# Kernel tuning notes

Measured on AMD Instinct MI355X. Metric: run time of the kernel, lower is better.

The kernel has to match this reference:

```python
import jax, jax.numpy as jnp
import numpy as np

NUM_TOKENS = 16384
HIDDEN = 2048
NUM_EXPERTS = 64
TOP_K = 2


def setup_inputs() -> dict:
    key = jax.random.key(0)
    kx, kw = jax.random.split(key)
    x = jax.random.normal(kx, (NUM_TOKENS, HIDDEN), dtype=jnp.float32)
    # nn.Linear weight is (num_experts, hidden); store transposed for x @ W
    W_gate = jax.random.normal(kw, (HIDDEN, NUM_EXPERTS), dtype=jnp.float32) * (1.0 / np.sqrt(HIDDEN))
    return {"x": x, "W_gate": W_gate}


def reference(x, W_gate):
    # gate matmul + softmax over experts
    logits = jnp.einsum("th,he->te", x, W_gate)          # (T, E)
    probs = jax.nn.softmax(logits, axis=-1)
    # top-k selection and renormalization
    top_k_weights, top_k_indices = jax.lax.top_k(probs, TOP_K)  # (T, k), (T, k)
    top_k_weights = top_k_weights / (jnp.sum(top_k_weights, axis=-1, keepdims=True) + 1e-9)
    # Switch-style load-balancing aux loss using top-1 assignments
    num_tokens = x.shape[0]
    top1 = top_k_indices[:, 0]
    tokens_per_expert = jnp.zeros((NUM_EXPERTS,), dtype=probs.dtype).at[top1].add(1.0)
    f = tokens_per_expert / num_tokens                    # fraction of tokens per expert
    P = jnp.mean(probs, axis=0)                           # mean router prob per expert
    aux_loss = NUM_EXPERTS * jnp.sum(f * P)
    return (top_k_weights, top_k_indices, aux_loss)
```

## Files before the change

### kernel.cpp

```cpp
#include <hip/hip_runtime.h>
#include <math.h>

#define NUM_TOKENS 16384
#define HIDDEN 2048
#define NUM_EXPERTS 64
#define TOPK 2

#define TM 64
#define KH 64
#define XS_STR 68

#define IDX_OFF 32768
#define AUX_OFF 65536

__global__ __launch_bounds__(256) void router_kernel(
    const float* __restrict__ x, const float* __restrict__ Wg,
    float* __restrict__ out, float* __restrict__ ws)
{
    __shared__ float sA[TM * XS_STR];
    __shared__ float sB[KH * NUM_EXPERTS];

    const int tid = threadIdx.x;
    const int bid = blockIdx.x;
    const int tx = tid & 15;
    const int ty = tid >> 4;
    const int tokBase = bid * TM;

    float C[4][4] = {{0.f,0.f,0.f,0.f},{0.f,0.f,0.f,0.f},{0.f,0.f,0.f,0.f},{0.f,0.f,0.f,0.f}};

    for (int hb = 0; hb < HIDDEN; hb += KH) {
        #pragma unroll
        for (int p = 0; p < 4; ++p) {
            int li = p * 256 + tid;
            int t  = li >> 4;
            int hq = li & 15;
            float4 v = *reinterpret_cast<const float4*>(
                &x[(size_t)(tokBase + t) * HIDDEN + hb + hq * 4]);
            *reinterpret_cast<float4*>(&sA[t * XS_STR + hq * 4]) = v;
        }
        #pragma unroll
        for (int p = 0; p < 4; ++p) {
            int li = p * 256 + tid;
            float4 v = *reinterpret_cast<const float4*>(
                &Wg[(size_t)hb * NUM_EXPERTS + li * 4]);
            *reinterpret_cast<float4*>(&sB[li * 4]) = v;
        }
        __syncthreads();

        #pragma unroll
        for (int k4 = 0; k4 < KH / 4; ++k4) {
            float xa[4][4];
            float wa[4][4];
            #pragma unroll
            for (int i = 0; i < 4; ++i) {
                float4 v = *reinterpret_cast<const float4*>(
                    &sA[(ty * 4 + i) * XS_STR + k4 * 4]);
                xa[i][0] = v.x; xa[i][1] = v.y; xa[i][2] = v.z; xa[i][3] = v.w;
            }
            #pragma unroll
            for (int kk = 0; kk < 4; ++kk) {
                float4 v = *reinterpret_cast<const float4*>(
                    &sB[(k4 * 4 + kk) * NUM_EXPERTS + tx * 4]);
                wa[kk][0] = v.x; wa[kk][1] = v.y; wa[kk][2] = v.z; wa[kk][3] = v.w;
            }
            #pragma unroll
            for (int i = 0; i < 4; ++i)
                #pragma unroll
                for (int kk = 0; kk < 4; ++kk)
                    #pragma unroll
                    for (int jj = 0; jj < 4; ++jj)
                        C[i][jj] = fmaf(xa[i][kk], wa[kk][jj], C[i][jj]);
        }
        __syncthreads();
    }

    #pragma unroll
    for (int i = 0; i < 4; ++i) {
        float4 v; v.x = C[i][0]; v.y = C[i][1]; v.z = C[i][2]; v.w = C[i][3];
        *reinterpret_cast<float4*>(&sA[(ty * 4 + i) * XS_STR + tx * 4]) = v;
    }
    __syncthreads();

    const int wave = tid >> 6;
    const int lane = tid & 63;
    float accP = 0.f;
    float accC = 0.f;

    for (int tt = 0; tt < TM / 4; ++tt) {
        int t = wave * (TM / 4) + tt;
        float l = sA[t * XS_STR + lane];

        float m = l;
        #pragma unroll
        for (int off = 32; off >= 1; off >>= 1) m = fmaxf(m, __shfl_xor(m, off));
        float p = expf(l - m);
        float Z = p;
        #pragma unroll
        for (int off = 32; off >= 1; off >>= 1) Z += __shfl_xor(Z, off);
        float prob = p / Z;

        float v1 = prob; int i1 = lane;
        #pragma unroll
        for (int off = 32; off >= 1; off >>= 1) {
            float ov = __shfl_xor(v1, off);
            int   oi = __shfl_xor(i1, off);
            if (ov > v1 || (ov == v1 && oi < i1)) { v1 = ov; i1 = oi; }
        }
        float v2 = (lane == i1) ? -1.f : prob; int i2 = lane;
        #pragma unroll
        for (int off = 32; off >= 1; off >>= 1) {
            float ov = __shfl_xor(v2, off);
            int   oi = __shfl_xor(i2, off);
            if (ov > v2 || (ov == v2 && oi < i2)) { v2 = ov; i2 = oi; }
        }

        accP += prob;
        if (lane == i1) accC += 1.f;

        if (lane == 0) {
            float s = v1 + v2 + 1e-9f;
            size_t o = (size_t)(tokBase + t) * 2;
            out[o]               = v1 / s;
            out[o + 1]           = v2 / s;
            out[IDX_OFF + o]     = (float)i1;
            out[IDX_OFF + o + 1] = (float)i2;
        }
    }

    sB[wave * 64 + lane]       = accP;
    sB[256 + wave * 64 + lane] = accC;
    __syncthreads();
    if (tid < 64) {
        float sp = sB[tid] + sB[64 + tid] + sB[128 + tid] + sB[192 + tid];
        float sc = sB[256 + tid] + sB[320 + tid] + sB[384 + tid] + sB[448 + tid];
        ws[(size_t)bid * 128 + tid]      = sp;
        ws[(size_t)bid * 128 + 64 + tid] = sc;
    }
}

__global__ __launch_bounds__(64) void finalize_kernel(
    const float* __restrict__ ws, float* __restrict__ out)
{
    int e = threadIdx.x;
    float sp = 0.f, sc = 0.f;
    for (int b = 0; b < NUM_TOKENS / TM; ++b) {
        sp += ws[(size_t)b * 128 + e];
        sc += ws[(size_t)b * 128 + 64 + e];
    }
    float val = (sc * (1.0f / NUM_TOKENS)) * (sp * (1.0f / NUM_TOKENS));
    #pragma unroll
    for (int off = 32; off >= 1; off >>= 1) val += __shfl_xor(val, off);
    if (e == 0) out[AUX_OFF] = (float)NUM_EXPERTS * val;
}

extern "C" void kernel_launch(void* const* d_in, const int* in_sizes, int n_in,
                              void* d_out, int out_size, void* d_ws, size_t ws_size,
                              hipStream_t stream) {
    const float* x  = (const float*)d_in[0];
    const float* Wg = (const float*)d_in[1];
    float* out = (float*)d_out;
    float* ws  = (float*)d_ws;

    router_kernel<<<NUM_TOKENS / TM, 256, 0, stream>>>(x, Wg, out, ws);
    finalize_kernel<<<1, 64, 0, stream>>>(ws, out);
}
```

Before: 116.6 us.

## Restructure router GEMM as per-token split-K with wave-uniform weight loads

Each thread now owns one token and accumulates all 64 expert logits in registers. Eight waves each take a 256-wide slice of the hidden dimension and read the gate weights with wave-uniform (scalar/broadcast) loads instead of staging them in shared memory. Partial sums are combined through a shared-memory tree reduction, and softmax/top-2 run per thread without cross-lane shuffles. The goal is to remove LDS staging and shuffle overhead. In exchange, x is read with strided per-thread rows (poor coalescing), register pressure rises (64 accumulators), and grid parallelism is limited to 256 blocks.

```diff
diff --git a/kernel.cpp b/kernel.cpp
--- a/kernel.cpp
+++ b/kernel.cpp
@@ -4,146 +4,132 @@
 #define NUM_TOKENS 16384
 #define HIDDEN 2048
 #define NUM_EXPERTS 64
-#define TOPK 2
-
-#define TM 64
-#define KH 64
-#define XS_STR 68
 
 #define IDX_OFF 32768
 #define AUX_OFF 65536
 
-__global__ __launch_bounds__(256) void router_kernel(
+#define KSLICE 256
+
+__global__ __launch_bounds__(512) void router_kernel(
     const float* __restrict__ x, const float* __restrict__ Wg,
     float* __restrict__ out, float* __restrict__ ws)
 {
-    __shared__ float sA[TM * XS_STR];
-    __shared__ float sB[KH * NUM_EXPERTS];
+    __shared__ float buf[4][64][68];
+    __shared__ int top1s[64];
 
-    const int tid = threadIdx.x;
-    const int bid = blockIdx.x;
-    const int tx = tid & 15;
-    const int ty = tid >> 4;
-    const int tokBase = bid * TM;
+    const int tid  = threadIdx.x;
+    const int w    = tid >> 6;
+    const int lane = tid & 63;
+    const int token = blockIdx.x * 64 + lane;
 
-    float C[4][4] = {{0.f,0.f,0.f,0.f},{0.f,0.f,0.f,0.f},{0.f,0.f,0.f,0.f},{0.f,0.f,0.f,0.f}};
+    const int k0 = __builtin_amdgcn_readfirstlane(w) * KSLICE;
 
-    for (int hb = 0; hb < HIDDEN; hb += KH) {
+    float C[64];
+    #pragma unroll
+    for (int e = 0; e < 64; ++e) C[e] = 0.f;
+
+    const float4* xr = reinterpret_cast<const float4*>(x + (size_t)token * HIDDEN + k0);
+
+    float4 xc[4], xn[4];
+    #pragma unroll
+    for (int j = 0; j < 4; ++j) xc[j] = xr[j];
+
+    for (int c = 0; c < 16; ++c) {
+        if (c < 15) {
+            #pragma unroll
+            for (int j = 0; j < 4; ++j) xn[j] = xr[(c + 1) * 4 + j];
+        }
+        const int kbase = k0 + c * 16;
         #pragma unroll
-        for (int p = 0; p < 4; ++p) {
-            int li = p * 256 + tid;
-            int t  = li >> 4;
-            int hq = li & 15;
-            float4 v = *reinterpret_cast<const float4*>(
-                &x[(size_t)(tokBase + t) * HIDDEN + hb + hq * 4]);
-            *reinterpret_cast<float4*>(&sA[t * XS_STR + hq * 4]) = v;
+        for (int j = 0; j < 4; ++j) {
+            const float xv[4] = {xc[j].x, xc[j].y, xc[j].z, xc[j].w};
+            #pragma unroll
+            for (int q = 0; q < 4; ++q) {
+                const int k = kbase + j * 4 + q;
+                const float4* wr = reinterpret_cast<const float4*>(Wg + (size_t)k * NUM_EXPERTS);
+                #pragma unroll
+                for (int e4 = 0; e4 < 16; ++e4) {
+                    const float4 wv = wr[e4];
+                    C[e4*4+0] = fmaf(xv[q], wv.x, C[e4*4+0]);
+                    C[e4*4+1] = fmaf(xv[q], wv.y, C[e4*4+1]);
+                    C[e4*4+2] = fmaf(xv[q], wv.z, C[e4*4+2]);
+                    C[e4*4+3] = fmaf(xv[q], wv.w, C[e4*4+3]);
+                }
+            }
         }
-        #pragma unroll
-        for (int p = 0; p < 4; ++p) {
-            int li = p * 256 + tid;
-            float4 v = *reinterpret_cast<const float4*>(
-                &Wg[(size_t)hb * NUM_EXPERTS + li * 4]);
-            *reinterpret_cast<float4*>(&sB[li * 4]) = v;
+        if (c < 15) {
+            #pragma unroll
+            for (int j = 0; j < 4; ++j) xc[j] = xn[j];
         }
-        __syncthreads();
-
-        #pragma unroll
-        for (int k4 = 0; k4 < KH / 4; ++k4) {
-            float xa[4][4];
-            float wa[4][4];
-            #pragma unroll
-            for (int i = 0; i < 4; ++i) {
-                float4 v = *reinterpret_cast<const float4*>(
-                    &sA[(ty * 4 + i) * XS_STR + k4 * 4]);
-                xa[i][0] = v.x; xa[i][1] = v.y; xa[i][2] = v.z; xa[i][3] = v.w;
-            }
-            #pragma unroll
-            for (int kk = 0; kk < 4; ++kk) {
-                float4 v = *reinterpret_cast<const float4*>(
-                    &sB[(k4 * 4 + kk) * NUM_EXPERTS + tx * 4]);
-                wa[kk][0] = v.x; wa[kk][1] = v.y; wa[kk][2] = v.z; wa[kk][3] = v.w;
-            }
-            #pragma unroll
-            for (int i = 0; i < 4; ++i)
-                #pragma unroll
-                for (int kk = 0; kk < 4; ++kk)
-                    #pragma unroll
-                    for (int jj = 0; jj < 4; ++jj)
-                        C[i][jj] = fmaf(xa[i][kk], wa[kk][jj], C[i][jj]);
-        }
-        __syncthreads();
     }
 
-    #pragma unroll
-    for (int i = 0; i < 4; ++i) {
-        float4 v; v.x = C[i][0]; v.y = C[i][1]; v.z = C[i][2]; v.w = C[i][3];
-        *reinterpret_cast<float4*>(&sA[(ty * 4 + i) * XS_STR + tx * 4]) = v;
+    #define WBUF(b) { _Pragma("unroll") for (int e4 = 0; e4 < 16; ++e4) { \
+        float4 v; v.x = C[e4*4+0]; v.y = C[e4*4+1]; v.z = C[e4*4+2]; v.w = C[e4*4+3]; \
+        *reinterpret_cast<float4*>(&buf[b][lane][e4*4]) = v; } }
+    #define ABUF(b) { _Pragma("unroll") for (int e4 = 0; e4 < 16; ++e4) { \
+        const float4 v = *reinterpret_cast<const float4*>(&buf[b][lane][e4*4]); \
+        C[e4*4+0] += v.x; C[e4*4+1] += v.y; C[e4*4+2] += v.z; C[e4*4+3] += v.w; } }
+
+    if (w >= 4) WBUF(w - 4);
+    __syncthreads();
+    if (w < 4) ABUF(w);
+    __syncthreads();
+    if (w == 2 || w == 3) WBUF(w - 2);
+    __syncthreads();
+    if (w < 2) ABUF(w);
+    __syncthreads();
+    if (w == 1) WBUF(0);
+    __syncthreads();
+
+    if (w == 0) {
+        ABUF(0);
+
+        float m = C[0];
+        #pragma unroll
+        for (int e = 1; e < 64; ++e) m = fmaxf(m, C[e]);
+        float Z = 0.f;
+        #pragma unroll
+        for (int e = 0; e < 64; ++e) { C[e] = expf(C[e] - m); Z += C[e]; }
+        const float rz = 1.f / Z;
+
+        float v1 = -1.f, v2 = -1.f; int i1 = 0, i2 = 0;
+        #pragma unroll
+        for (int e = 0; e < 64; ++e) {
+            const float p = C[e] * rz;
+            C[e] = p;
+            if (p > v1)      { v2 = v1; i2 = i1; v1 = p; i1 = e; }
+            else if (p > v2) { v2 = p;  i2 = e; }
+        }
+
+        const float s = v1 + v2 + 1e-9f;
+        float2 wo; wo.x = v1 / s; wo.y = v2 / s;
+        *reinterpret_cast<float2*>(&out[(size_t)token * 2]) = wo;
+        float2 io; io.x = (float)i1; io.y = (float)i2;
+        *reinterpret_cast<float2*>(&out[IDX_OFF + (size_t)token * 2]) = io;
+
+        WBUF(0);
+        top1s[lane] = i1;
     }
     __syncthreads();
 
-    const int wave = tid >> 6;
-    const int lane = tid & 63;
-    float accP = 0.f;
-    float accC = 0.f;
-
-    for (int tt = 0; tt < TM / 4; ++tt) {
-        int t = wave * (TM / 4) + tt;
-        float l = sA[t * XS_STR + lane];
-
-        float m = l;
-        #pragma unroll
-        for (int off = 32; off >= 1; off >>= 1) m = fmaxf(m, __shfl_xor(m, off));
-        float p = expf(l - m);
-        float Z = p;
-        #pragma unroll
-        for (int off = 32; off >= 1; off >>= 1) Z += __shfl_xor(Z, off);
-        float prob = p / Z;
-
-        float v1 = prob; int i1 = lane;
-        #pragma unroll
-        for (int off = 32; off >= 1; off >>= 1) {
-            float ov = __shfl_xor(v1, off);
-            int   oi = __shfl_xor(i1, off);
-            if (ov > v1 || (ov == v1 && oi < i1)) { v1 = ov; i1 = oi; }
-        }
-        float v2 = (lane == i1) ? -1.f : prob; int i2 = lane;
-        #pragma unroll
-        for (int off = 32; off >= 1; off >>= 1) {
-            float ov = __shfl_xor(v2, off);
-            int   oi = __shfl_xor(i2, off);
-            if (ov > v2 || (ov == v2 && oi < i2)) { v2 = ov; i2 = oi; }
-        }
-
-        accP += prob;
-        if (lane == i1) accC += 1.f;
-
-        if (lane == 0) {
-            float s = v1 + v2 + 1e-9f;
-            size_t o = (size_t)(tokBase + t) * 2;
-            out[o]               = v1 / s;
-            out[o + 1]           = v2 / s;
-            out[IDX_OFF + o]     = (float)i1;
-            out[IDX_OFF + o + 1] = (float)i2;
-        }
-    }
-
-    sB[wave * 64 + lane]       = accP;
-    sB[256 + wave * 64 + lane] = accC;
-    __syncthreads();
-    if (tid < 64) {
-        float sp = sB[tid] + sB[64 + tid] + sB[128 + tid] + sB[192 + tid];
-        float sc = sB[256 + tid] + sB[320 + tid] + sB[384 + tid] + sB[448 + tid];
-        ws[(size_t)bid * 128 + tid]      = sp;
-        ws[(size_t)bid * 128 + 64 + tid] = sc;
+    if (w == 1) {
+        float sp = 0.f;
+        #pragma unroll 8
+        for (int t = 0; t < 64; ++t) sp += buf[0][t][lane];
+        float cnt = 0.f;
+        #pragma unroll 8
+        for (int t = 0; t < 64; ++t) cnt += (top1s[t] == lane) ? 1.f : 0.f;
+        ws[(size_t)blockIdx.x * 128 + lane]      = sp;
+        ws[(size_t)blockIdx.x * 128 + 64 + lane] = cnt;
     }
 }
 
 __global__ __launch_bounds__(64) void finalize_kernel(
     const float* __restrict__ ws, float* __restrict__ out)
 {
-    int e = threadIdx.x;
+    const int e = threadIdx.x;
     float sp = 0.f, sc = 0.f;
-    for (int b = 0; b < NUM_TOKENS / TM; ++b) {
+    for (int b = 0; b < NUM_TOKENS / 64; ++b) {
         sp += ws[(size_t)b * 128 + e];
         sc += ws[(size_t)b * 128 + 64 + e];
     }
@@ -161,6 +147,6 @@
     float* out = (float*)d_out;
     float* ws  = (float*)d_ws;
 
-    router_kernel<<<NUM_TOKENS / TM, 256, 0, stream>>>(x, Wg, out, ws);
+    router_kernel<<<NUM_TOKENS / 64, 512, 0, stream>>>(x, Wg, out, ws);
     finalize_kernel<<<1, 64, 0, stream>>>(ws, out);
 }
```

Result: slower. 345.8 us (+196.6%).
